# Kernel optimization log

Hardware: AMD Instinct MI355X
Metric: run time of the kernel (lower is better)

The kernel has to match this reference:

```python
import jax, jax.numpy as jnp
import numpy as np

N_E = 2048
E_DIM = 128
BETA = 0.25

def setup_inputs() -> dict:
    key = jax.random.key(0)
    k1, k2 = jax.random.split(key)
    z = jax.random.normal(k1, (16, 2048, E_DIM), dtype=jnp.float32)
    # nn.Embedding weight init: uniform(-1/n_e, 1/n_e)
    emb = jax.random.uniform(k2, (N_E, E_DIM), dtype=jnp.float32,
                             minval=-1.0 / N_E, maxval=1.0 / N_E)
    return {"z": z, "emb": emb}

def reference(z, emb):
    beta = BETA
    zf = z.reshape(-1, E_DIM)                      # [M, e_dim]
    # d = ||z||^2 + ||e||^2 - 2 z e^T  -> [M, n_e]
    d = (jnp.sum(zf * zf, axis=1, keepdims=True)
         + jnp.sum(emb * emb, axis=1)
         - 2.0 * jnp.einsum('md,nd->mn', zf, emb))
    idx = jnp.argmin(d, axis=1)                    # [M]
    min_encodings = jax.nn.one_hot(idx, N_E, dtype=z.dtype)  # [M, n_e]
    # one-hot @ emb == direct gather
    z_q = jnp.take(emb, idx, axis=0).reshape(z.shape)
    sg = jax.lax.stop_gradient
    loss = jnp.mean((sg(z_q) - z) ** 2) + beta * jnp.mean((z_q - sg(z)) ** 2)
    z_q_st = z + sg(z_q - z)                       # straight-through
    e_mean = jnp.mean(min_encodings, axis=0)
    perplexity = jnp.exp(-jnp.sum(e_mean * jnp.log(e_mean + 1e-10)))
    return (loss, z_q_st, perplexity, min_encodings, idx[:, None])
```

## Files before the change

kernel.cpp:

```cpp
#include <hip/hip_runtime.h>
#include <hip/hip_bf16.h>
#include <hip/hip_fp16.h>
#include <math.h>

#define M_ROWS 32768
#define NE 2048
#define EDIM 128

#define O_LOSS 0
#define O_ZQ 1
#define O_PERP 4194305
#define O_MINENC 4194306
#define O_IDX 71303170ll

#define AS1 __attribute__((address_space(1)))
#define AS3 __attribute__((address_space(3)))

typedef unsigned short u16;
typedef __attribute__((ext_vector_type(8))) _Float16 half8;
typedef __attribute__((ext_vector_type(16))) float f32x16;

#define ZPLANE2 4194304

__device__ __forceinline__ void gload16u(const u16* g, u16* l) {
    __builtin_amdgcn_global_load_lds((const AS1 void*)g, (AS3 void*)l, 16, 0, 0);
}

__global__ __launch_bounds__(256) void prep_kernel(const float* __restrict__ z,
                                                   const float* __restrict__ emb,
                                                   u16* __restrict__ z2,
                                                   u16* __restrict__ e2p,
                                                   float* __restrict__ zsums) {
    const int tid = threadIdx.x;
    const int rl = tid >> 4;
    const int sub = tid & 15;
    const int b = blockIdx.x;

    if (b < 2048) {
        const int row = b * 16 + rl;
        const float* zr = z + (size_t)row * EDIM + sub * 8;
        float4 v0 = reinterpret_cast<const float4*>(zr)[0];
        float4 v1 = reinterpret_cast<const float4*>(zr)[1];
        float fv[8] = {v0.x, v0.y, v0.z, v0.w, v1.x, v1.y, v1.z, v1.w};
        u16 hs[8], ms[8];
        float s = 0.0f;
        #pragma unroll
        for (int j = 0; j < 8; j++) {
            s += fv[j] * fv[j];
            __half hh = __float2half_rn(fv[j]);
            float fh = __half2float(hh);
            float r = fv[j] - fh;
            __half hm = __float2half_rn(r);
            hs[j] = __half_as_ushort(hh);
            ms[j] = __half_as_ushort(hm);
        }
        size_t off = (size_t)row * EDIM + sub * 8;
        reinterpret_cast<ushort4*>(z2 + off)[0] = make_ushort4(hs[0], hs[1], hs[2], hs[3]);
        reinterpret_cast<ushort4*>(z2 + off + 4)[0] = make_ushort4(hs[4], hs[5], hs[6], hs[7]);
        reinterpret_cast<ushort4*>(z2 + (size_t)ZPLANE2 + off)[0] = make_ushort4(ms[0], ms[1], ms[2], ms[3]);
        reinterpret_cast<ushort4*>(z2 + (size_t)ZPLANE2 + off + 4)[0] = make_ushort4(ms[4], ms[5], ms[6], ms[7]);
        #pragma unroll
        for (int o = 8; o >= 1; o >>= 1) s += __shfl_xor(s, o);
        if (sub == 0) zsums[row] = s;
    } else {
        const int n = (b - 2048) * 16 + rl;
        const float* er = emb + (size_t)n * EDIM + sub * 8;
        float4 v0 = reinterpret_cast<const float4*>(er)[0];
        float4 v1 = reinterpret_cast<const float4*>(er)[1];
        float fv[8] = {v0.x * 2048.0f, v0.y * 2048.0f, v0.z * 2048.0f, v0.w * 2048.0f,
                       v1.x * 2048.0f, v1.y * 2048.0f, v1.z * 2048.0f, v1.w * 2048.0f};
        u16 hs[8], ms[8];
        #pragma unroll
        for (int j = 0; j < 8; j++) {
            __half hh = __float2half_rn(fv[j]);
            float fh = __half2float(hh);
            float r = fv[j] - fh;
            __half hm = __float2half_rn(r);
            hs[j] = __half_as_ushort(hh);
            ms[j] = __half_as_ushort(hm);
        }
        const int strip = n >> 5, r32n = n & 31;
        const int jj2 = sub >> 1, hh2 = sub & 1;
        size_t base = ((size_t)(strip * 8 + jj2) * 2) * 512 + (size_t)(hh2 * 32 + r32n) * 8;
        reinterpret_cast<ushort4*>(e2p + base)[0]       = make_ushort4(hs[0], hs[1], hs[2], hs[3]);
        reinterpret_cast<ushort4*>(e2p + base + 4)[0]   = make_ushort4(hs[4], hs[5], hs[6], hs[7]);
        reinterpret_cast<ushort4*>(e2p + base + 512)[0] = make_ushort4(ms[0], ms[1], ms[2], ms[3]);
        reinterpret_cast<ushort4*>(e2p + base + 516)[0] = make_ushort4(ms[4], ms[5], ms[6], ms[7]);
    }
}

__global__ void eq_kernel(const float* __restrict__ emb, float* __restrict__ eq,
                          int* __restrict__ hist) {
    int n = blockIdx.x;
    int lane = threadIdx.x;
    float v0 = emb[(size_t)n * EDIM + lane];
    float v1 = emb[(size_t)n * EDIM + 64 + lane];
    float s = v0 * v0 + v1 * v1;
    #pragma unroll
    for (int off = 32; off >= 1; off >>= 1) s += __shfl_down(s, off);
    if (lane == 0) { eq[n] = s; hist[n] = 0; }
}

template<int WE>
__global__ __launch_bounds__(256, 2) void argmin_mfma_kernel(
    const u16* __restrict__ z2, const u16* __restrict__ e2p,
    const float* __restrict__ zsums, const float* __restrict__ eq,
    int* __restrict__ out_idx, float* __restrict__ out, int* __restrict__ hist,
    const float* __restrict__ z, const float* __restrict__ emb,
    float* __restrict__ part)
{
    __shared__ __align__(16) u16 zs[16384];
    __shared__ float zsl[64];
    __shared__ float cand_v[256];
    __shared__ int   cand_i[256];
    __shared__ int   ids[64];
    __shared__ float red[256];

    const int tid = threadIdx.x;
    const int w = tid >> 6, l = tid & 63;
    const int wn = w;
    const int h = l >> 5, r32 = l & 31;
    const int m0 = blockIdx.x * 64;

    #pragma unroll
    for (int jj = 0; jj < 8; jj++) {
        int s0 = jj * 256 + w * 64;
        int s = s0 + l;
        int lv = s >> 10, kc = (s >> 6) & 15, row = s & 63;
        gload16u(z2 + (size_t)lv * ZPLANE2 + ((size_t)(m0 + row) << 7) + kc * 8,
                 zs + s0 * 8);
    }
    if (tid < 64) zsl[tid] = zsums[m0 + tid];
    __syncthreads();

    float best[2][16];
    int   bidx[2][16];
    #pragma unroll
    for (int i2 = 0; i2 < 2; i2++)
        #pragma unroll
        for (int q = 0; q < 16; q++) { best[i2][q] = 3.4e38f; bidx[i2][q] = 0; }

    float2* me2 = reinterpret_cast<float2*>(out + O_MINENC + (size_t)m0 * NE);

    for (int tt = 0; tt < 16; tt++) {
        if constexpr (WE) {
            const float2 zz2 = make_float2(0.0f, 0.0f);
            #pragma unroll
            for (int j = 0; j < 16; j++)
                me2[tt * 4096 + j * 256 + tid] = zz2;
        }

        f32x16 am[2], ac[2];
        #pragma unroll
        for (int i2 = 0; i2 < 2; i2++)
            #pragma unroll
            for (int q = 0; q < 16; q++) { am[i2][q] = 0.0f; ac[i2][q] = 0.0f; }

        const int strip = tt * 4 + wn;
        const u16* bb = e2p + ((size_t)strip * 16) * 512 + (size_t)l * 8;

        #pragma unroll 4
        for (int j = 0; j < 8; j++) {
            half8 b0 = *reinterpret_cast<const half8*>(bb + (size_t)(j * 2 + 0) * 512);
            half8 b1 = *reinterpret_cast<const half8*>(bb + (size_t)(j * 2 + 1) * 512);
            half8 a00 = *reinterpret_cast<const half8*>(zs + ((0 * 16 + j * 2 + h) * 64 + 0 * 32 + r32) * 8);
            half8 a01 = *reinterpret_cast<const half8*>(zs + ((1 * 16 + j * 2 + h) * 64 + 0 * 32 + r32) * 8);
            half8 a10 = *reinterpret_cast<const half8*>(zs + ((0 * 16 + j * 2 + h) * 64 + 1 * 32 + r32) * 8);
            half8 a11 = *reinterpret_cast<const half8*>(zs + ((1 * 16 + j * 2 + h) * 64 + 1 * 32 + r32) * 8);

            am[0] = __builtin_amdgcn_mfma_f32_32x32x16_f16(a00, b0, am[0], 0, 0, 0);
            ac[0] = __builtin_amdgcn_mfma_f32_32x32x16_f16(a00, b1, ac[0], 0, 0, 0);
            ac[0] = __builtin_amdgcn_mfma_f32_32x32x16_f16(a01, b0, ac[0], 0, 0, 0);
            am[1] = __builtin_amdgcn_mfma_f32_32x32x16_f16(a10, b0, am[1], 0, 0, 0);
            ac[1] = __builtin_amdgcn_mfma_f32_32x32x16_f16(a10, b1, ac[1], 0, 0, 0);
            ac[1] = __builtin_amdgcn_mfma_f32_32x32x16_f16(a11, b0, ac[1], 0, 0, 0);
        }

        const int n = tt * 128 + wn * 32 + r32;
        const float eqv = eq[n];
        #pragma unroll
        for (int i2 = 0; i2 < 2; i2++) {
            #pragma unroll
            for (int q = 0; q < 16; q++) {
                const int row = i2 * 32 + ((q & 3) + 8 * (q >> 2) + 4 * h);
                float zse = zsl[row] + eqv;
                float dotp = am[i2][q] + ac[i2][q];
                float val = zse - dotp * 0.0009765625f;
                if (val < best[i2][q]) { best[i2][q] = val; bidx[i2][q] = n; }
            }
        }
    }

    #pragma unroll
    for (int off = 16; off >= 1; off >>= 1) {
        #pragma unroll
        for (int i2 = 0; i2 < 2; i2++)
            #pragma unroll
            for (int q = 0; q < 16; q++) {
                float ov = __shfl_xor(best[i2][q], off);
                int   oi = __shfl_xor(bidx[i2][q], off);
                if (ov < best[i2][q] || (ov == best[i2][q] && oi < bidx[i2][q])) {
                    best[i2][q] = ov; bidx[i2][q] = oi;
                }
            }
    }
    if (r32 == 0) {
        #pragma unroll
        for (int i2 = 0; i2 < 2; i2++)
            #pragma unroll
            for (int q = 0; q < 16; q++) {
                int row = i2 * 32 + ((q & 3) + 8 * (q >> 2) + 4 * h);
                cand_v[row * 4 + wn] = best[i2][q];
                cand_i[row * 4 + wn] = bidx[i2][q];
            }
    }
    __syncthreads();
    if (tid < 64) {
        float bv = cand_v[tid * 4 + 0];
        int   bi = cand_i[tid * 4 + 0];
        #pragma unroll
        for (int j = 1; j < 4; j++) {
            float v = cand_v[tid * 4 + j];
            int   ii = cand_i[tid * 4 + j];
            if (v < bv || (v == bv && ii < bi)) { bv = v; bi = ii; }
        }
        ids[tid] = bi;
        out_idx[m0 + tid] = bi;
        out[O_IDX + m0 + tid] = (float)bi;
        atomicAdd(&hist[bi], 1);
        if constexpr (WE)
            out[O_MINENC + (size_t)(m0 + tid) * NE + bi] = 1.0f;
    }
    __syncthreads();

    float s = 0.0f;
    #pragma unroll
    for (int j = 0; j < 4; j++) {
        int u = j * 256 + tid;
        int r = u >> 4, sub = u & 15;
        int id = ids[r];
        const float* zr = z + (size_t)(m0 + r) * EDIM + sub * 8;
        const float* er = emb + (size_t)id * EDIM + sub * 8;
        float* outr = out + O_ZQ + (size_t)(m0 + r) * EDIM + sub * 8;
        float4 z0 = reinterpret_cast<const float4*>(zr)[0];
        float4 z1 = reinterpret_cast<const float4*>(zr)[1];
        float4 e0 = reinterpret_cast<const float4*>(er)[0];
        float4 e1 = reinterpret_cast<const float4*>(er)[1];
        float zz[8] = {z0.x, z0.y, z0.z, z0.w, z1.x, z1.y, z1.z, z1.w};
        float ee[8] = {e0.x, e0.y, e0.z, e0.w, e1.x, e1.y, e1.z, e1.w};
        #pragma unroll
        for (int jj = 0; jj < 8; jj++) {
            float d = ee[jj] - zz[jj];
            outr[jj] = zz[jj] + d;
            s += d * d;
        }
    }
    red[tid] = s;
    __syncthreads();
    #pragma unroll
    for (int o = 128; o >= 1; o >>= 1) {
        if (tid < o) red[tid] += red[tid + o];
        __syncthreads();
    }
    if (tid == 0) part[blockIdx.x] = red[0];
}

__global__ __launch_bounds__(256) void minenc_kernel(const int* __restrict__ idx,
                                                     float* __restrict__ out) {
    size_t i = (size_t)blockIdx.x * blockDim.x + threadIdx.x;
    const size_t total = (size_t)M_ROWS * (NE / 2);
    const size_t stride = (size_t)gridDim.x * blockDim.x;
    for (; i < total; i += stride) {
        int row = (int)(i >> 10);
        int col = (int)(i & 1023) << 1;
        int id = idx[row];
        float2 v;
        v.x = (col == id) ? 1.0f : 0.0f;
        v.y = (col + 1 == id) ? 1.0f : 0.0f;
        reinterpret_cast<float2*>(out)[i] = v;
    }
}

__global__ __launch_bounds__(256) void finalize_kernel(const float* __restrict__ partial,
                                                       const int* __restrict__ hist,
                                                       float* __restrict__ out) {
    __shared__ float red[256];
    const int tid = threadIdx.x;
    float s = partial[tid] + partial[tid + 256];
    red[tid] = s;
    __syncthreads();
    #pragma unroll
    for (int o = 128; o >= 1; o >>= 1) {
        if (tid < o) red[tid] += red[tid + o];
        __syncthreads();
    }
    if (tid == 0) out[O_LOSS] = 1.25f * red[0] / (float)((size_t)M_ROWS * EDIM);
    __syncthreads();

    float h = 0.0f;
    for (int i = 0; i < 8; i++) {
        float p = (float)hist[tid * 8 + i] * (1.0f / (float)M_ROWS);
        h += p * logf(p + 1e-10f);
    }
    red[tid] = h;
    __syncthreads();
    #pragma unroll
    for (int o = 128; o >= 1; o >>= 1) {
        if (tid < o) red[tid] += red[tid + o];
        __syncthreads();
    }
    if (tid == 0) out[O_PERP] = expf(-red[0]);
}

extern "C" void kernel_launch(void* const* d_in, const int* in_sizes, int n_in,
                              void* d_out, int out_size, void* d_ws, size_t ws_size,
                              hipStream_t stream) {
    const float* z   = (const float*)d_in[0];
    const float* emb = (const float*)d_in[1];
    float* out = (float*)d_out;

    char* ws = (char*)d_ws;
    float* eq    = (float*)ws;
    int*   idx   = (int*)(ws + 8192);
    int*   hist  = (int*)(ws + 139264);
    float* part  = (float*)(ws + 147456);
    float* zsums = (float*)(ws + 155648);

    const bool big_ws = (ws_size >= (size_t)(40u << 20));
    u16 *Z2, *E2P;
    if (big_ws) {
        Z2  = (u16*)(ws + (4u << 20));
        E2P = (u16*)(ws + (24u << 20));
    } else {
        Z2  = (u16*)(out + O_MINENC + 2);
        E2P = Z2 + 2 * (size_t)ZPLANE2;
    }

    prep_kernel<<<2176, 256, 0, stream>>>(z, emb, Z2, E2P, zsums);
    eq_kernel<<<NE, 64, 0, stream>>>(emb, eq, hist);
    if (big_ws) {
        argmin_mfma_kernel<1><<<512, 256, 0, stream>>>(Z2, E2P, zsums, eq, idx, out, hist, z, emb, part);
    } else {
        argmin_mfma_kernel<0><<<512, 256, 0, stream>>>(Z2, E2P, zsums, eq, idx, out, hist, z, emb, part);
        minenc_kernel<<<8192, 256, 0, stream>>>(idx, out + O_MINENC);
    }
    finalize_kernel<<<1, 256, 0, stream>>>(part, hist, out);
}
```

Measured before the change: 118.8 us.

## Fuse z fp16 split into argmin kernel and prefetch codebook fragments

The separate prep pass that wrote the z hi/lo fp16 planes and row norms to global memory is removed. The argmin kernel now loads fp32 z directly, splits it into LDS and computes row norms in-block. Codebook preparation is merged with the norm kernel into one launch. The MFMA loop now register-double-buffers the next B fragments, and the one-hot zero stores are moved after the MFMA loop. This saves a global round trip and a launch, but adds conversion work inside the main kernel and raises register pressure.

```diff
diff --git a/kernel.cpp b/kernel.cpp
--- a/kernel.cpp
+++ b/kernel.cpp
@@ -13,40 +13,29 @@
 #define O_MINENC 4194306
 #define O_IDX 71303170ll
 
-#define AS1 __attribute__((address_space(1)))
-#define AS3 __attribute__((address_space(3)))
-
 typedef unsigned short u16;
 typedef __attribute__((ext_vector_type(8))) _Float16 half8;
+typedef __attribute__((ext_vector_type(8))) unsigned short ushort8;
 typedef __attribute__((ext_vector_type(16))) float f32x16;
 
-#define ZPLANE2 4194304
-
-__device__ __forceinline__ void gload16u(const u16* g, u16* l) {
-    __builtin_amdgcn_global_load_lds((const AS1 void*)g, (AS3 void*)l, 16, 0, 0);
-}
-
-__global__ __launch_bounds__(256) void prep_kernel(const float* __restrict__ z,
-                                                   const float* __restrict__ emb,
-                                                   u16* __restrict__ z2,
-                                                   u16* __restrict__ e2p,
-                                                   float* __restrict__ zsums) {
-    const int tid = threadIdx.x;
-    const int rl = tid >> 4;
-    const int sub = tid & 15;
-    const int b = blockIdx.x;
-
-    if (b < 2048) {
-        const int row = b * 16 + rl;
-        const float* zr = z + (size_t)row * EDIM + sub * 8;
-        float4 v0 = reinterpret_cast<const float4*>(zr)[0];
-        float4 v1 = reinterpret_cast<const float4*>(zr)[1];
-        float fv[8] = {v0.x, v0.y, v0.z, v0.w, v1.x, v1.y, v1.z, v1.w};
-        u16 hs[8], ms[8];
-        float s = 0.0f;
-        #pragma unroll
-        for (int j = 0; j < 8; j++) {
-            s += fv[j] * fv[j];
+__global__ void prep_e_kernel(const float* __restrict__ emb, float* __restrict__ eq,
+                              int* __restrict__ hist, u16* __restrict__ e2p) {
+    const int n = blockIdx.x;
+    const int lane = threadIdx.x;
+    float v0 = emb[(size_t)n * EDIM + lane];
+    float v1 = emb[(size_t)n * EDIM + 64 + lane];
+    float s = v0 * v0 + v1 * v1;
+    #pragma unroll
+    for (int off = 32; off >= 1; off >>= 1) s += __shfl_down(s, off);
+    if (lane == 0) { eq[n] = s; hist[n] = 0; }
+
+    if (lane < 32) {
+        const int k = lane * 4;
+        float4 e4 = reinterpret_cast<const float4*>(emb + (size_t)n * EDIM + k)[0];
+        float fv[4] = {e4.x * 2048.0f, e4.y * 2048.0f, e4.z * 2048.0f, e4.w * 2048.0f};
+        u16 hs[4], ms[4];
+        #pragma unroll
+        for (int j = 0; j < 4; j++) {
             __half hh = __float2half_rn(fv[j]);
             float fh = __half2float(hh);
             float r = fv[j] - fh;
@@ -54,57 +43,17 @@
             hs[j] = __half_as_ushort(hh);
             ms[j] = __half_as_ushort(hm);
         }
-        size_t off = (size_t)row * EDIM + sub * 8;
-        reinterpret_cast<ushort4*>(z2 + off)[0] = make_ushort4(hs[0], hs[1], hs[2], hs[3]);
-        reinterpret_cast<ushort4*>(z2 + off + 4)[0] = make_ushort4(hs[4], hs[5], hs[6], hs[7]);
-        reinterpret_cast<ushort4*>(z2 + (size_t)ZPLANE2 + off)[0] = make_ushort4(ms[0], ms[1], ms[2], ms[3]);
-        reinterpret_cast<ushort4*>(z2 + (size_t)ZPLANE2 + off + 4)[0] = make_ushort4(ms[4], ms[5], ms[6], ms[7]);
-        #pragma unroll
-        for (int o = 8; o >= 1; o >>= 1) s += __shfl_xor(s, o);
-        if (sub == 0) zsums[row] = s;
-    } else {
-        const int n = (b - 2048) * 16 + rl;
-        const float* er = emb + (size_t)n * EDIM + sub * 8;
-        float4 v0 = reinterpret_cast<const float4*>(er)[0];
-        float4 v1 = reinterpret_cast<const float4*>(er)[1];
-        float fv[8] = {v0.x * 2048.0f, v0.y * 2048.0f, v0.z * 2048.0f, v0.w * 2048.0f,
-                       v1.x * 2048.0f, v1.y * 2048.0f, v1.z * 2048.0f, v1.w * 2048.0f};
-        u16 hs[8], ms[8];
-        #pragma unroll
-        for (int j = 0; j < 8; j++) {
-            __half hh = __float2half_rn(fv[j]);
-            float fh = __half2float(hh);
-            float r = fv[j] - fh;
-            __half hm = __float2half_rn(r);
-            hs[j] = __half_as_ushort(hh);
-            ms[j] = __half_as_ushort(hm);
-        }
         const int strip = n >> 5, r32n = n & 31;
-        const int jj2 = sub >> 1, hh2 = sub & 1;
-        size_t base = ((size_t)(strip * 8 + jj2) * 2) * 512 + (size_t)(hh2 * 32 + r32n) * 8;
+        const int jj = k >> 4, hh2 = (k >> 3) & 1, slot4 = k & 7;
+        size_t base = ((size_t)(strip * 8 + jj) * 2) * 512 + (size_t)(hh2 * 32 + r32n) * 8 + slot4;
         reinterpret_cast<ushort4*>(e2p + base)[0]       = make_ushort4(hs[0], hs[1], hs[2], hs[3]);
-        reinterpret_cast<ushort4*>(e2p + base + 4)[0]   = make_ushort4(hs[4], hs[5], hs[6], hs[7]);
         reinterpret_cast<ushort4*>(e2p + base + 512)[0] = make_ushort4(ms[0], ms[1], ms[2], ms[3]);
-        reinterpret_cast<ushort4*>(e2p + base + 516)[0] = make_ushort4(ms[4], ms[5], ms[6], ms[7]);
-    }
-}
-
-__global__ void eq_kernel(const float* __restrict__ emb, float* __restrict__ eq,
-                          int* __restrict__ hist) {
-    int n = blockIdx.x;
-    int lane = threadIdx.x;
-    float v0 = emb[(size_t)n * EDIM + lane];
-    float v1 = emb[(size_t)n * EDIM + 64 + lane];
-    float s = v0 * v0 + v1 * v1;
-    #pragma unroll
-    for (int off = 32; off >= 1; off >>= 1) s += __shfl_down(s, off);
-    if (lane == 0) { eq[n] = s; hist[n] = 0; }
+    }
 }
 
 template<int WE>
 __global__ __launch_bounds__(256, 2) void argmin_mfma_kernel(
-    const u16* __restrict__ z2, const u16* __restrict__ e2p,
-    const float* __restrict__ zsums, const float* __restrict__ eq,
+    const u16* __restrict__ e2p, const float* __restrict__ eq,
     int* __restrict__ out_idx, float* __restrict__ out, int* __restrict__ hist,
     const float* __restrict__ z, const float* __restrict__ emb,
     float* __restrict__ part)
@@ -122,15 +71,33 @@
     const int h = l >> 5, r32 = l & 31;
     const int m0 = blockIdx.x * 64;
 
-    #pragma unroll
-    for (int jj = 0; jj < 8; jj++) {
-        int s0 = jj * 256 + w * 64;
-        int s = s0 + l;
-        int lv = s >> 10, kc = (s >> 6) & 15, row = s & 63;
-        gload16u(z2 + (size_t)lv * ZPLANE2 + ((size_t)(m0 + row) << 7) + kc * 8,
-                 zs + s0 * 8);
-    }
-    if (tid < 64) zsl[tid] = zsums[m0 + tid];
+    float zsp = 0.0f;
+    #pragma unroll
+    for (int p = 0; p < 4; p++) {
+        const int s = p * 256 + tid;
+        const int row = s & 63;
+        const int kc = s >> 6;
+        const float* zp = z + (size_t)(m0 + row) * EDIM + kc * 8;
+        float4 u0 = reinterpret_cast<const float4*>(zp)[0];
+        float4 u1 = reinterpret_cast<const float4*>(zp)[1];
+        float f[8] = {u0.x, u0.y, u0.z, u0.w, u1.x, u1.y, u1.z, u1.w};
+        ushort8 hv, mv;
+        #pragma unroll
+        for (int j = 0; j < 8; j++) {
+            zsp += f[j] * f[j];
+            __half hh = __float2half_rn(f[j]);
+            float fh = __half2float(hh);
+            float r = f[j] - fh;
+            __half hm = __float2half_rn(r);
+            hv[j] = __half_as_ushort(hh);
+            mv[j] = __half_as_ushort(hm);
+        }
+        *reinterpret_cast<ushort8*>(zs + (size_t)s * 8) = hv;
+        *reinterpret_cast<ushort8*>(zs + 8192 + (size_t)s * 8) = mv;
+    }
+    red[tid] = zsp;
+    __syncthreads();
+    if (tid < 64) zsl[tid] = red[tid] + red[tid + 64] + red[tid + 128] + red[tid + 192];
     __syncthreads();
 
     float best[2][16];
@@ -142,13 +109,14 @@
 
     float2* me2 = reinterpret_cast<float2*>(out + O_MINENC + (size_t)m0 * NE);
 
+    const u16* bb = e2p + ((size_t)(0 * 4 + wn) * 16) * 512 + (size_t)l * 8;
+    half8 nb0 = *reinterpret_cast<const half8*>(bb);
+    half8 nb1 = *reinterpret_cast<const half8*>(bb + 512);
+
     for (int tt = 0; tt < 16; tt++) {
-        if constexpr (WE) {
-            const float2 zz2 = make_float2(0.0f, 0.0f);
-            #pragma unroll
-            for (int j = 0; j < 16; j++)
-                me2[tt * 4096 + j * 256 + tid] = zz2;
-        }
+        bb = e2p + ((size_t)(tt * 4 + wn) * 16) * 512 + (size_t)l * 8;
+        const int n = tt * 128 + wn * 32 + r32;
+        const float eqv = eq[n];
 
         f32x16 am[2], ac[2];
         #pragma unroll
@@ -156,28 +124,37 @@
             #pragma unroll
             for (int q = 0; q < 16; q++) { am[i2][q] = 0.0f; ac[i2][q] = 0.0f; }
 
-        const int strip = tt * 4 + wn;
-        const u16* bb = e2p + ((size_t)strip * 16) * 512 + (size_t)l * 8;
-
-        #pragma unroll 4
+        #pragma unroll
         for (int j = 0; j < 8; j++) {
-            half8 b0 = *reinterpret_cast<const half8*>(bb + (size_t)(j * 2 + 0) * 512);
-            half8 b1 = *reinterpret_cast<const half8*>(bb + (size_t)(j * 2 + 1) * 512);
+            half8 cb0 = nb0, cb1 = nb1;
+            if (j < 7) {
+                nb0 = *reinterpret_cast<const half8*>(bb + (size_t)(j + 1) * 1024);
+                nb1 = *reinterpret_cast<const half8*>(bb + (size_t)(j + 1) * 1024 + 512);
+            } else if (tt < 15) {
+                const u16* nbb = e2p + ((size_t)((tt + 1) * 4 + wn) * 16) * 512 + (size_t)l * 8;
+                nb0 = *reinterpret_cast<const half8*>(nbb);
+                nb1 = *reinterpret_cast<const half8*>(nbb + 512);
+            }
             half8 a00 = *reinterpret_cast<const half8*>(zs + ((0 * 16 + j * 2 + h) * 64 + 0 * 32 + r32) * 8);
             half8 a01 = *reinterpret_cast<const half8*>(zs + ((1 * 16 + j * 2 + h) * 64 + 0 * 32 + r32) * 8);
             half8 a10 = *reinterpret_cast<const half8*>(zs + ((0 * 16 + j * 2 + h) * 64 + 1 * 32 + r32) * 8);
             half8 a11 = *reinterpret_cast<const half8*>(zs + ((1 * 16 + j * 2 + h) * 64 + 1 * 32 + r32) * 8);
 
-            am[0] = __builtin_amdgcn_mfma_f32_32x32x16_f16(a00, b0, am[0], 0, 0, 0);
-            ac[0] = __builtin_amdgcn_mfma_f32_32x32x16_f16(a00, b1, ac[0], 0, 0, 0);
-            ac[0] = __builtin_amdgcn_mfma_f32_32x32x16_f16(a01, b0, ac[0], 0, 0, 0);
-            am[1] = __builtin_amdgcn_mfma_f32_32x32x16_f16(a10, b0, am[1], 0, 0, 0);
-            ac[1] = __builtin_amdgcn_mfma_f32_32x32x16_f16(a10, b1, ac[1], 0, 0, 0);
-            ac[1] = __builtin_amdgcn_mfma_f32_32x32x16_f16(a11, b0, ac[1], 0, 0, 0);
-        }
-
-        const int n = tt * 128 + wn * 32 + r32;
-        const float eqv = eq[n];
+            am[0] = __builtin_amdgcn_mfma_f32_32x32x16_f16(a00, cb0, am[0], 0, 0, 0);
+            ac[0] = __builtin_amdgcn_mfma_f32_32x32x16_f16(a00, cb1, ac[0], 0, 0, 0);
+            ac[0] = __builtin_amdgcn_mfma_f32_32x32x16_f16(a01, cb0, ac[0], 0, 0, 0);
+            am[1] = __builtin_amdgcn_mfma_f32_32x32x16_f16(a10, cb0, am[1], 0, 0, 0);
+            ac[1] = __builtin_amdgcn_mfma_f32_32x32x16_f16(a10, cb1, ac[1], 0, 0, 0);
+            ac[1] = __builtin_amdgcn_mfma_f32_32x32x16_f16(a11, cb0, ac[1], 0, 0, 0);
+        }
+
+        if constexpr (WE) {
+            const float2 zz2 = make_float2(0.0f, 0.0f);
+            #pragma unroll
+            for (int jj = 0; jj < 16; jj++)
+                me2[tt * 4096 + jj * 256 + tid] = zz2;
+        }
+
         #pragma unroll
         for (int i2 = 0; i2 < 2; i2++) {
             #pragma unroll
@@ -324,24 +301,20 @@
     int*   idx   = (int*)(ws + 8192);
     int*   hist  = (int*)(ws + 139264);
     float* part  = (float*)(ws + 147456);
-    float* zsums = (float*)(ws + 155648);
-
-    const bool big_ws = (ws_size >= (size_t)(40u << 20));
-    u16 *Z2, *E2P;
+
+    const bool big_ws = (ws_size >= (size_t)(8u << 20));
+    u16* E2P;
     if (big_ws) {
-        Z2  = (u16*)(ws + (4u << 20));
-        E2P = (u16*)(ws + (24u << 20));
+        E2P = (u16*)(ws + (4u << 20));
     } else {
-        Z2  = (u16*)(out + O_MINENC + 2);
-        E2P = Z2 + 2 * (size_t)ZPLANE2;
-    }
-
-    prep_kernel<<<2176, 256, 0, stream>>>(z, emb, Z2, E2P, zsums);
-    eq_kernel<<<NE, 64, 0, stream>>>(emb, eq, hist);
+        E2P = (u16*)(out + O_MINENC + 2);
+    }
+
+    prep_e_kernel<<<NE, 64, 0, stream>>>(emb, eq, hist, E2P);
     if (big_ws) {
-        argmin_mfma_kernel<1><<<512, 256, 0, stream>>>(Z2, E2P, zsums, eq, idx, out, hist, z, emb, part);
+        argmin_mfma_kernel<1><<<512, 256, 0, stream>>>(E2P, eq, idx, out, hist, z, emb, part);
     } else {
-        argmin_mfma_kernel<0><<<512, 256, 0, stream>>>(Z2, E2P, zsums, eq, idx, out, hist, z, emb, part);
+        argmin_mfma_kernel<0><<<512, 256, 0, stream>>>(E2P, eq, idx, out, hist, z, emb, part);
         minenc_kernel<<<8192, 256, 0, stream>>>(idx, out + O_MINENC);
     }
     finalize_kernel<<<1, 256, 0, stream>>>(part, hist, out);
```

Measured after the change: 170.1 us. +43.2%, slower.
